# Optimization experiments

Measured on AMD Instinct MI355X. Metric: run time of the kernel, lower is better.

The kernel has to match this reference:

```python
import jax, jax.numpy as jnp
import numpy as np

B, T, F = 512, 1024, 8
H1, H2 = 70, 21   # '80k' config, bidirectional
D1, D2 = 30, 20


def _u(key, shape, fan):
    s = 1.0 / np.sqrt(fan)
    return jax.random.uniform(key, shape, jnp.float32, -s, s)


def setup_inputs() -> dict:
    key = jax.random.key(0)
    ks = iter(jax.random.split(key, 32))
    inp = {"x": jax.random.normal(next(ks), (B, T, F), jnp.float32)}
    # LSTM layer 1 (input F -> H1), forward and backward directions; torch gate order i,f,g,o
    for d in ("f", "b"):
        inp[f"w_ih1_{d}"] = _u(next(ks), (4 * H1, F), H1)
        inp[f"w_hh1_{d}"] = _u(next(ks), (4 * H1, H1), H1)
        inp[f"b_ih1_{d}"] = _u(next(ks), (4 * H1,), H1)
        inp[f"b_hh1_{d}"] = _u(next(ks), (4 * H1,), H1)
    # LSTM layer 2 (input 2*H1 -> H2)
    for d in ("f", "b"):
        inp[f"w_ih2_{d}"] = _u(next(ks), (4 * H2, 2 * H1), H2)
        inp[f"w_hh2_{d}"] = _u(next(ks), (4 * H2, H2), H2)
        inp[f"b_ih2_{d}"] = _u(next(ks), (4 * H2,), H2)
        inp[f"b_hh2_{d}"] = _u(next(ks), (4 * H2,), H2)
    # Dense head: 2*H2 -> D1 -> D2 -> 1
    inp["d1_w"] = _u(next(ks), (D1, 2 * H2), 2 * H2)
    inp["d1_b"] = _u(next(ks), (D1,), 2 * H2)
    inp["d2_w"] = _u(next(ks), (D2, D1), D1)
    inp["d2_b"] = _u(next(ks), (D2,), D1)
    inp["out_w"] = _u(next(ks), (1, D2), D2)
    inp["out_b"] = _u(next(ks), (1,), D2)
    return inp


def _lstm_dir(x, w_ih, w_hh, b_ih, b_hh, reverse):
    # x: [B, T, Fin]; torch LSTM gate order: i, f, g, o
    if reverse:
        x = x[:, ::-1]
    H = w_hh.shape[1]
    pre = jnp.einsum('btf,gf->btg', x, w_ih) + b_ih + b_hh  # [B, T, 4H]
    pre_t = jnp.moveaxis(pre, 1, 0)                          # [T, B, 4H]

    def step(carry, p):
        h, c = carry
        g = p + h @ w_hh.T
        i, f, gg, o = jnp.split(g, 4, axis=-1)
        c = jax.nn.sigmoid(f) * c + jax.nn.sigmoid(i) * jnp.tanh(gg)
        h = jax.nn.sigmoid(o) * jnp.tanh(c)
        return (h, c), h

    init = (jnp.zeros((x.shape[0], H), x.dtype), jnp.zeros((x.shape[0], H), x.dtype))
    _, hs = jax.lax.scan(step, init, pre_t)
    hs = jnp.moveaxis(hs, 0, 1)  # [B, T, H]
    if reverse:
        hs = hs[:, ::-1]
    return hs


def _bilstm(x, wf, uf, bif, bhf, wb, ub, bib, bhb):
    return jnp.concatenate([
        _lstm_dir(x, wf, uf, bif, bhf, reverse=False),
        _lstm_dir(x, wb, ub, bib, bhb, reverse=True),
    ], axis=-1)


def reference(x,
              w_ih1_f, w_hh1_f, b_ih1_f, b_hh1_f,
              w_ih1_b, w_hh1_b, b_ih1_b, b_hh1_b,
              w_ih2_f, w_hh2_f, b_ih2_f, b_hh2_f,
              w_ih2_b, w_hh2_b, b_ih2_b, b_hh2_b,
              d1_w, d1_b, d2_w, d2_b, out_w, out_b):
    h = _bilstm(x, w_ih1_f, w_hh1_f, b_ih1_f, b_hh1_f,
                w_ih1_b, w_hh1_b, b_ih1_b, b_hh1_b)   # [B, T, 2*H1]
    h = _bilstm(h, w_ih2_f, w_hh2_f, b_ih2_f, b_hh2_f,
                w_ih2_b, w_hh2_b, b_ih2_b, b_hh2_b)   # [B, T, 2*H2]
    h = jax.nn.relu(h @ d1_w.T + d1_b)
    h = jax.nn.relu(h @ d2_w.T + d2_b)
    return h @ out_w.T + out_b                          # [B, T, 1]
```

## Files before the change

### kernel.cpp

```cpp
#include <hip/hip_runtime.h>


typedef _Float16 v2f16 __attribute__((ext_vector_type(2)));
typedef _Float16 v4h   __attribute__((ext_vector_type(4)));
typedef _Float16 v8h   __attribute__((ext_vector_type(8)));
typedef float    f32x4 __attribute__((ext_vector_type(4)));

__device__ __forceinline__ float fdot2(v2f16 a, v2f16 b, float c) {
  return __builtin_amdgcn_fdot2(a, b, c, false);
}
#if __has_builtin(__builtin_amdgcn_rcpf)
__device__ __forceinline__ float rcpf(float x) { return __builtin_amdgcn_rcpf(x); }
#else
__device__ __forceinline__ float rcpf(float x) { return 1.f / x; }
#endif
__device__ __forceinline__ float ex2(float v) {
#if __has_builtin(__builtin_amdgcn_exp2f)
  return __builtin_amdgcn_exp2f(v);
#else
  return __expf(v * 0.6931471805599453f);
#endif
}
__device__ __forceinline__ float dpp_xor1(float v) {
  return __builtin_bit_cast(float,
      __builtin_amdgcn_update_dpp(0, __builtin_bit_cast(int, v),
                                  0xB1 , 0xF, 0xF, true));
}

__device__ __forceinline__ void lds_barrier() {
  asm volatile("s_waitcnt lgkmcnt(0)" ::: "memory");
  __builtin_amdgcn_s_barrier();
  __builtin_amdgcn_sched_barrier(0);
}

#define LOG2E  1.4426950408889634f
#define LOG2E2 2.8853900817779268f

#define O_W1M  0u
#define O_WP2  110592u
#define O_W2M  118656u
#define O_BIAS 177792u
#define O_DATA 178496u

__global__ void pack_kernel(const float* __restrict__ wihf, const float* __restrict__ whhf,
                            const float* __restrict__ wihb, const float* __restrict__ whhb,
                            const float* __restrict__ b1if, const float* __restrict__ b1hf,
                            const float* __restrict__ b1ib, const float* __restrict__ b1hb,
                            const float* __restrict__ wih2f, const float* __restrict__ wih2b,
                            const float* __restrict__ whh2f, const float* __restrict__ whh2b,
                            const float* __restrict__ bif, const float* __restrict__ bhf,
                            const float* __restrict__ bib, const float* __restrict__ bhb,
                            char* __restrict__ ws) {
  _Float16* w1m = (_Float16*)(ws + O_W1M);
  _Float16* wp2 = (_Float16*)(ws + O_WP2);
  _Float16* w2m = (_Float16*)(ws + O_W2M);
  float* biasc = (float*)(ws + O_BIAS);
  int idx = blockIdx.x * 256 + threadIdx.x;
  if (idx < 55296) {
    int d = idx / 27648, rem = idx % 27648, rp = rem / 96, k = rem % 96;
    int u = rp >> 2, g = rp & 3;
    const float* wih = d ? wihb : wihf;
    const float* whh = d ? whhb : whhf;
    const float* bi = d ? b1ib : b1if;
    const float* bh = d ? b1hb : b1hf;
    float v = 0.f;
    if (u < 70) {
      int src = g * 70 + u;
      float scale = (g == 2) ? LOG2E2 : LOG2E;
      if (k < 8) v = wih[src * 8 + k] * scale;
      else if (k < 78) v = whh[src * 70 + (k - 8)] * scale;
      else if (k == 78) v = (bi[src] + bh[src]) * scale;
    }
    w1m[idx] = (_Float16)v;
  } else if (idx < 59328) {
    int j = idx - 55296;
    int d = j / 2016, rem = j % 2016, r = rem / 24, k = rem % 24;
    const float* whh = d ? whh2b : whh2f;
    float scale = (r / 21 == 2) ? LOG2E2 : LOG2E;
    wp2[j] = (_Float16)((k < 21) ? whh[r * 21 + k] * scale : 0.f);
  } else if (idx < 88896) {
    int j = idx - 59328;
    int n = j / 168, k = j % 168;
    float v = 0.f;
    if (n < 168 && k < 140) {
      int d = n / 84, m = n % 84, u = m >> 2, g = m & 3;
      const float* wih = d ? wih2b : wih2f;
      float scale = (g == 2) ? LOG2E2 : LOG2E;
      v = wih[(g * 21 + u) * 140 + k] * scale;
    }
    w2m[j] = (_Float16)v;
  } else if (idx < 89072) {
    int n = idx - 88896;
    float v = 0.f;
    if (n < 168) {
      int d = n / 84, m = n % 84, u = m >> 2, g = m & 3;
      const float* bi = d ? bib : bif;
      const float* bh = d ? bhb : bhf;
      float scale = (g == 2) ? LOG2E2 : LOG2E;
      v = (bi[g * 21 + u] + bh[g * 21 + u]) * scale;
    }
    biasc[n] = v;
  }
}

__global__ __launch_bounds__(1024) void lstm1_kernel(
    const float* __restrict__ x,
    const _Float16* __restrict__ w1m,
    _Float16* __restrict__ h1, int b0, int nb) {
  __shared__ __align__(16) _Float16 km[2][16][104];
  const int tid = threadIdx.x;
  const int w = tid >> 6, lane = tid & 63;
  const int q = lane >> 4, bc = lane & 15;
  const int d = blockIdx.y;
  const int blg = blockIdx.x * 16;
  const int gb0 = b0 + blg;

  for (int i = tid; i < 2 * 16 * 104; i += 1024) ((_Float16*)km)[i] = (_Float16)0.f;

  const bool ldr = (w == 15);
  const bool two = (w < 2) || (w == 14);
  const int T0 = (w < 2) ? 2 * w : (w == 14 ? 16 : w + 2);

  v8h af[2][3];
  if (!ldr) {
#pragma unroll
    for (int kc = 0; kc < 3; ++kc)
      af[0][kc] = *(const v8h*)&w1m[(size_t)(d * 288 + T0 * 16 + bc) * 96 + kc * 32 + q * 8];
    if (two) {
#pragma unroll
      for (int kc = 0; kc < 3; ++kc)
        af[1][kc] = *(const v8h*)&w1m[(size_t)(d * 288 + (T0 + 1) * 16 + bc) * 96 + kc * 32 + q * 8];
    }
  }

  __syncthreads();

  if (tid < 16) {
    km[0][tid][78] = (_Float16)1.f;
    km[1][tid][78] = (_Float16)1.f;
  }
  const bool xlane = ldr && (lane < 32);
  const int xb = lane >> 1, xhalf = lane & 1;
  float4 xa, xb4, xc, xd;
  const float* xp = nullptr;
  const ptrdiff_t xstep = d ? -8 : 8;
  if (xlane) {
    const float* xrow = &x[((size_t)(gb0 + xb) * 1024) * 8 + xhalf * 4];
    int t0 = d ? 1023 : 0;
    float4 xv = *(const float4*)&xrow[(size_t)t0 * 8];
    v4h xh; xh[0] = (_Float16)xv.x; xh[1] = (_Float16)xv.y;
    xh[2] = (_Float16)xv.z; xh[3] = (_Float16)xv.w;
    *(v4h*)&km[0][xb][xhalf * 4] = xh;
    xa  = *(const float4*)&xrow[(size_t)(d ? 1022 : 1) * 8];
    xb4 = *(const float4*)&xrow[(size_t)(d ? 1021 : 2) * 8];
    xc  = *(const float4*)&xrow[(size_t)(d ? 1020 : 3) * 8];
    xd  = *(const float4*)&xrow[(size_t)(d ? 1019 : 4) * 8];
    xp  = &xrow[(size_t)(d ? 1018 : 5) * 8];
  }
  float c0 = 0.f, c1 = 0.f;
  int s = 0;
  __syncthreads();

#define GATE(Ai, ci, U)                                                      \
    {                                                                        \
      float ei = ex2(-Ai[0]);                                                \
      float ef = ex2(-Ai[1]);                                                \
      float eg = ex2(-Ai[2]);                                                \
      float eo = ex2(-Ai[3]);                                                \
      float sf = rcpf(1.f + ef);                                             \
      float ig = (1.f - eg) * rcpf((1.f + ei) * (1.f + eg));                 \
      ci = fmaf(sf, ci, ig);                                                 \
      float cl = fminf(fmaxf(ci, -14.f), 14.f);                              \
      float ec = ex2(cl * -LOG2E2);                                          \
      float hv = (1.f - ec) * rcpf((1.f + eo) * (1.f + ec));                 \
      if ((U) < 70) {                                                        \
        _Float16 hh = (_Float16)hv;                                          \
        km[nxt][bc][8 + (U)] = hh;                                           \
        h1[rowb + (U)] = hh;                                                 \
      }                                                                      \
    }

#define STEP1(XR)                                                            \
  {                                                                          \
    const int cur = s & 1, nxt = cur ^ 1;                                    \
    if (!ldr) {                                                              \
      v8h bf0 = *(const v8h*)&km[cur][bc][q * 8];                            \
      v8h bf1 = *(const v8h*)&km[cur][bc][32 + q * 8];                       \
      v8h bf2 = *(const v8h*)&km[cur][bc][64 + q * 8];                       \
      f32x4 z4 = (f32x4){0.f, 0.f, 0.f, 0.f};                                \
      f32x4 A0 = __builtin_amdgcn_mfma_f32_16x16x32_f16(af[0][0], bf0, z4, 0, 0, 0); \
      f32x4 A1 = z4;                                                         \
      if (two) A1 = __builtin_amdgcn_mfma_f32_16x16x32_f16(af[1][0], bf0, z4, 0, 0, 0); \
      A0 = __builtin_amdgcn_mfma_f32_16x16x32_f16(af[0][1], bf1, A0, 0, 0, 0); \
      if (two) A1 = __builtin_amdgcn_mfma_f32_16x16x32_f16(af[1][1], bf1, A1, 0, 0, 0); \
      A0 = __builtin_amdgcn_mfma_f32_16x16x32_f16(af[0][2], bf2, A0, 0, 0, 0); \
      if (two) A1 = __builtin_amdgcn_mfma_f32_16x16x32_f16(af[1][2], bf2, A1, 0, 0, 0); \
      const int te = d ? (1023 - s) : s;                                     \
      const size_t rowb = ((size_t)te * nb + blg + bc) * 176 + d * 70;       \
      GATE(A0, c0, T0 * 4 + q)                                               \
      if (two) GATE(A1, c1, (T0 + 1) * 4 + q)                                \
    } else if (xlane) {                                                      \
      if (s < 1023) {                                                        \
        v4h xh; xh[0] = (_Float16)XR.x; xh[1] = (_Float16)XR.y;              \
        xh[2] = (_Float16)XR.z; xh[3] = (_Float16)XR.w;                      \
        *(v4h*)&km[nxt][xb][xhalf * 4] = xh;                                 \
      }                                                                      \
      if (s <= 1018) XR = *(const float4*)xp;                                \
      xp += xstep;                                                           \
    }                                                                        \
    ++s;                                                                     \
    lds_barrier();                                                           \
  }

#pragma unroll 1
  for (int it = 0; it < 256; ++it) {
    STEP1(xa)
    STEP1(xb4)
    STEP1(xc)
    STEP1(xd)
  }
#undef STEP1
#undef GATE
}

__global__ __launch_bounds__(256) void pre2_kernel(
    _Float16* __restrict__ h1, const char* __restrict__ ws) {
  const _Float16* w2m = (const _Float16*)(ws + O_W2M);
  const float* biasc = (const float*)(ws + O_BIAS);
  __shared__ _Float16 Al[64][184];
  __shared__ float Bl[176];
  const int tid = threadIdx.x;
  const int r0 = blockIdx.x * 64;
#pragma unroll
  for (int i = 0; i < 6; ++i) {
    int cid = i * 256 + tid;
    if (cid < 1408) {
      int row = cid / 22, ch = cid % 22;
      *(v8h*)&Al[row][ch * 8] = *(const v8h*)&h1[(size_t)(r0 + row) * 176 + ch * 8];
    }
  }
  if (tid < 176) Bl[tid] = biasc[tid];
  __syncthreads();

  const int wv = tid >> 6, lane = tid & 63;
  const int ml = lane & 15, kq = lane >> 4;
  v8h af[5];
#pragma unroll
  for (int k = 0; k < 4; ++k)
    af[k] = *(const v8h*)&Al[wv * 16 + ml][k * 32 + kq * 8];
  {
    v8h a4 = *(const v8h*)&Al[wv * 16 + ml][128 + kq * 8];
    if (kq >= 2) {
#pragma unroll
      for (int j = 0; j < 8; ++j) a4[j] = (_Float16)0.f;
    } else if (kq == 1) {
#pragma unroll
      for (int j = 4; j < 8; ++j) a4[j] = (_Float16)0.f;
    }
    af[4] = a4;
  }

  const v8h* wg = (const v8h*)w2m;
  f32x4 acc[11];
#pragma unroll
  for (int ct = 0; ct < 11; ++ct) acc[ct] = (f32x4){0.f, 0.f, 0.f, 0.f};

  v8h bc[5], bn[5];
#pragma unroll
  for (int k = 0; k < 5; ++k) bn[k] = wg[(size_t)ml * 21 + k * 4 + kq];
#pragma unroll
  for (int ct = 0; ct < 11; ++ct) {
#pragma unroll
    for (int k = 0; k < 5; ++k) bc[k] = bn[k];
    if (ct < 10) {
#pragma unroll
      for (int k = 0; k < 5; ++k) bn[k] = wg[(size_t)((ct + 1) * 16 + ml) * 21 + k * 4 + kq];
    }
#pragma unroll
    for (int k = 0; k < 5; ++k)
      acc[ct] = __builtin_amdgcn_mfma_f32_16x16x32_f16(af[k], bc[k], acc[ct], 0, 0, 0);
  }
  __syncthreads();
#pragma unroll
  for (int ct = 0; ct < 11; ++ct) {
#pragma unroll
    for (int r = 0; r < 4; ++r) {
      int row = wv * 16 + kq * 4 + r, col = ct * 16 + ml;
      Al[row][col] = (_Float16)(acc[ct][r] + Bl[col]);
    }
  }
  __syncthreads();
#pragma unroll
  for (int i = 0; i < 6; ++i) {
    int cid = i * 256 + tid;
    if (cid < 1408) {
      int row = cid / 22, ch = cid % 22;
      *(v8h*)&h1[(size_t)(r0 + row) * 176 + ch * 8] = *(const v8h*)&Al[row][ch * 8];
    }
  }
}

__global__ __launch_bounds__(64) void lstm2_kernel(
    const _Float16* __restrict__ pre2, const _Float16* __restrict__ wp2,
    _Float16* __restrict__ h2, int nb) {
  __shared__ __align__(16) _Float16 kv[2][32];
  const int lane = threadIdx.x;
  const int bl = blockIdx.x;
  const int d = blockIdx.y;
  const int u = lane >> 1, p = lane & 1;
  const bool active = lane < 42;

  ((_Float16*)kv)[lane] = (_Float16)0.f;

  v2f16 w0[12], w1[12];
  if (active) {
    const v8h* wr0 = (const v8h*)&wp2[(d * 84 + (2 * p) * 21 + u) * 24];
    const v8h* wr1 = (const v8h*)&wp2[(d * 84 + (2 * p + 1) * 21 + u) * 24];
#pragma unroll
    for (int ch = 0; ch < 3; ++ch) {
      v8h a = wr0[ch], b = wr1[ch];
#pragma unroll
      for (int q = 0; q < 4; ++q) {
        v2f16 t0; t0[0] = a[2 * q]; t0[1] = a[2 * q + 1]; w0[ch * 4 + q] = t0;
        v2f16 t1; t1[0] = b[2 * q]; t1[1] = b[2 * q + 1]; w1[ch * 4 + q] = t1;
      }
    }
  }
  const int cp = d * 84 + u * 4 + 2 * p;
  const ptrdiff_t dlt = (ptrdiff_t)(d ? -nb : nb) * 176;
  const _Float16* pp = pre2 + ((size_t)(d ? 1023 : 0) * (size_t)nb + bl) * 176;

  v2f16 pa = *(const v2f16*)(pp + cp);
  v2f16 pb = *(const v2f16*)(pp + dlt + cp);
  v2f16 pc = *(const v2f16*)(pp + 2 * dlt + cp);
  v2f16 pd = *(const v2f16*)(pp + 3 * dlt + cp);
  v2f16 pe = *(const v2f16*)(pp + 4 * dlt + cp);
  v2f16 pg = *(const v2f16*)(pp + 5 * dlt + cp);
  v2f16 ph = *(const v2f16*)(pp + 6 * dlt + cp);
  v2f16 pi = *(const v2f16*)(pp + 7 * dlt + cp);
  const _Float16* pf = pp + 8 * dlt;

  float cc = 0.f;
  int s = 0;

#define L2STEP(P)                                                           \
  {                                                                         \
    const int cur = s & 1, nxt = cur ^ 1;                                   \
    float A0v = (float)P[0], A1v = (float)P[1];                             \
    const float4* kp = (const float4*)&kv[cur][0];                          \
    float4 q0 = kp[0], q1 = kp[1], q2 = kp[2];                              \
    __builtin_amdgcn_s_setprio(1);                                          \
    float x0 = A0v, x1 = 0.f, x2 = 0.f, x3 = 0.f;                           \
    float z0 = A1v, z1 = 0.f, z2 = 0.f, z3 = 0.f;                           \
    x0 = fdot2(__builtin_bit_cast(v2f16, q0.x), w0[0], x0);                 \
    x1 = fdot2(__builtin_bit_cast(v2f16, q0.y), w0[1], x1);                 \
    x2 = fdot2(__builtin_bit_cast(v2f16, q0.z), w0[2], x2);                 \
    x3 = fdot2(__builtin_bit_cast(v2f16, q0.w), w0[3], x3);                 \
    x0 = fdot2(__builtin_bit_cast(v2f16, q1.x), w0[4], x0);                 \
    x1 = fdot2(__builtin_bit_cast(v2f16, q1.y), w0[5], x1);                 \
    x2 = fdot2(__builtin_bit_cast(v2f16, q1.z), w0[6], x2);                 \
    x3 = fdot2(__builtin_bit_cast(v2f16, q1.w), w0[7], x3);                 \
    x0 = fdot2(__builtin_bit_cast(v2f16, q2.x), w0[8], x0);                 \
    x1 = fdot2(__builtin_bit_cast(v2f16, q2.y), w0[9], x1);                 \
    x2 = fdot2(__builtin_bit_cast(v2f16, q2.z), w0[10], x2);                \
    x3 = fdot2(__builtin_bit_cast(v2f16, q2.w), w0[11], x3);                \
    z0 = fdot2(__builtin_bit_cast(v2f16, q0.x), w1[0], z0);                 \
    z1 = fdot2(__builtin_bit_cast(v2f16, q0.y), w1[1], z1);                 \
    z2 = fdot2(__builtin_bit_cast(v2f16, q0.z), w1[2], z2);                 \
    z3 = fdot2(__builtin_bit_cast(v2f16, q0.w), w1[3], z3);                 \
    z0 = fdot2(__builtin_bit_cast(v2f16, q1.x), w1[4], z0);                 \
    z1 = fdot2(__builtin_bit_cast(v2f16, q1.y), w1[5], z1);                 \
    z2 = fdot2(__builtin_bit_cast(v2f16, q1.z), w1[6], z2);                 \
    z3 = fdot2(__builtin_bit_cast(v2f16, q1.w), w1[7], z3);                 \
    z0 = fdot2(__builtin_bit_cast(v2f16, q2.x), w1[8], z0);                 \
    z1 = fdot2(__builtin_bit_cast(v2f16, q2.y), w1[9], z1);                 \
    z2 = fdot2(__builtin_bit_cast(v2f16, q2.z), w1[10], z2);                \
    z3 = fdot2(__builtin_bit_cast(v2f16, q2.w), w1[11], z3);                \
    float A = (x0 + x1) + (x2 + x3), Bv = (z0 + z1) + (z2 + z3);            \
            \
    float r0v = rcpf(1.f + ex2(-A));                                        \
    float Y0 = p ? fmaf(2.f, r0v, -1.f) : r0v;                              \
    float Y1 = rcpf(1.f + ex2(-Bv));                                        \
    float Zs = dpp_xor1(Y0);                                                \
    float Ws = dpp_xor1(Y1);                                                \
    float ai = p ? Zs : Y0;                                                 \
    float af = p ? Ws : Y1;                                                 \
    float ag = p ? Y0 : Zs;                                                 \
    float ao = p ? Y1 : Ws;                                                 \
    cc = fmaf(af, cc, ai * ag);                                             \
    float tc = fmaf(2.f, rcpf(1.f + ex2(cc * -LOG2E2)), -1.f);              \
    float hv = ao * tc;                                                     \
    __builtin_amdgcn_s_setprio(0);                                          \
    if (active && p == 0) {                                                 \
      _Float16 hh = (_Float16)hv;                                           \
      int te = d ? (1023 - s) : s;                                          \
      kv[nxt][u] = hh;                                                      \
      h2[((size_t)te * nb + bl) * 48 + d * 21 + u] = hh;                    \
    }                                                                       \
    if (s < 1016) P = *(const v2f16*)(pf + cp);                             \
    pf += dlt;                                                              \
    ++s;                                                                    \
  }

#pragma unroll 1
  for (int it = 0; it < 128; ++it) {
    L2STEP(pa)
    L2STEP(pb)
    L2STEP(pc)
    L2STEP(pd)
    L2STEP(pe)
    L2STEP(pg)
    L2STEP(ph)
    L2STEP(pi)
  }
#undef L2STEP
}

__global__ __launch_bounds__(256) void head_kernel(
    const _Float16* __restrict__ h2,
    const float* __restrict__ d1w, const float* __restrict__ d1b,
    const float* __restrict__ d2w, const float* __restrict__ d2b,
    const float* __restrict__ ow, const float* __restrict__ ob,
    float* __restrict__ out, int b0, int lognb) {
  int n = blockIdx.x * 256 + threadIdx.x;
  int t = n >> lognb, bl = n & ((1 << lognb) - 1);
  const v8h* hp = (const v8h*)&h2[(size_t)n * 48];
  float in[48];
#pragma unroll
  for (int i = 0; i < 6; ++i) {
    v8h hc = hp[i];
#pragma unroll
    for (int j = 0; j < 8; ++j) in[i * 8 + j] = (float)hc[j];
  }
  float a1[30];
#pragma unroll
  for (int cc = 0; cc < 30; ++cc) {
    float a = d1b[cc];
#pragma unroll
    for (int k = 0; k < 42; ++k) a += in[k] * d1w[cc * 42 + k];
    a1[cc] = fmaxf(a, 0.f);
  }
  float a2[20];
#pragma unroll
  for (int cc = 0; cc < 20; ++cc) {
    float a = d2b[cc];
#pragma unroll
    for (int k = 0; k < 30; ++k) a += a1[k] * d2w[cc * 30 + k];
    a2[cc] = fmaxf(a, 0.f);
  }
  float o = ob[0];
#pragma unroll
  for (int k = 0; k < 20; ++k) o += a2[k] * ow[k];
  out[(size_t)(b0 + bl) * 1024 + t] = o;
}

extern "C" void kernel_launch(void* const* d_in, const int* in_sizes, int n_in,
                              void* d_out, int out_size, void* d_ws, size_t ws_size,
                              hipStream_t stream) {
  const float* x = (const float*)d_in[0];
  const float* wih1f = (const float*)d_in[1];
  const float* whh1f = (const float*)d_in[2];
  const float* bih1f = (const float*)d_in[3];
  const float* bhh1f = (const float*)d_in[4];
  const float* wih1b = (const float*)d_in[5];
  const float* whh1b = (const float*)d_in[6];
  const float* bih1b = (const float*)d_in[7];
  const float* bhh1b = (const float*)d_in[8];
  const float* wih2f = (const float*)d_in[9];
  const float* whh2f = (const float*)d_in[10];
  const float* bih2f = (const float*)d_in[11];
  const float* bhh2f = (const float*)d_in[12];
  const float* wih2b = (const float*)d_in[13];
  const float* whh2b = (const float*)d_in[14];
  const float* bih2b = (const float*)d_in[15];
  const float* bhh2b = (const float*)d_in[16];
  const float* d1w = (const float*)d_in[17];
  const float* d1b = (const float*)d_in[18];
  const float* d2w = (const float*)d_in[19];
  const float* d2b = (const float*)d_in[20];
  const float* ow = (const float*)d_in[21];
  const float* ob = (const float*)d_in[22];
  float* out = (float*)d_out;
  char* wsb = (char*)d_ws;

  const int cands[6] = {1, 2, 4, 8, 16, 32};
  int nslice = 32;
  for (int i = 0; i < 6; ++i) {
    size_t rows = (size_t)(512 / cands[i]) * 1024;
    if (O_DATA + rows * 448 <= ws_size) { nslice = cands[i]; break; }
  }
  const int nb = 512 / nslice;
  int lognb = 0; while ((1 << lognb) < nb) ++lognb;
  const size_t rows = (size_t)nb * 1024;

  _Float16* w1m = (_Float16*)(wsb + O_W1M);
  _Float16* wp2 = (_Float16*)(wsb + O_WP2);
  _Float16* h1  = (_Float16*)(wsb + O_DATA);
  _Float16* h2  = (_Float16*)(wsb + O_DATA + rows * 352);

  pack_kernel<<<348, 256, 0, stream>>>(wih1f, whh1f, wih1b, whh1b,
                                       bih1f, bhh1f, bih1b, bhh1b,
                                       wih2f, wih2b, whh2f, whh2b,
                                       bih2f, bhh2f, bih2b, bhh2b, wsb);

  for (int s = 0; s < nslice; ++s) {
    const int b0 = s * nb;
    lstm1_kernel<<<dim3(nb / 16, 2), 1024, 0, stream>>>(x, w1m, h1, b0, nb);
    pre2_kernel<<<nb * 16, 256, 0, stream>>>(h1, wsb);
    lstm2_kernel<<<dim3(nb, 2), 64, 0, stream>>>(h1, wp2, h2, nb);
    head_kernel<<<nb * 4, 256, 0, stream>>>(h2, d1w, d1b, d2w, d2b, ow, ob,
                                            out, b0, lognb);
  }
}
```

Measured before the change: 1.199 ms.

## Fuse layer-2 input projection into layer-1 recurrence via atomic fp16 accumulation

```diff
diff --git a/kernel.cpp b/kernel.cpp
--- a/kernel.cpp
+++ b/kernel.cpp
@@ -1,4 +1,5 @@
 #include <hip/hip_runtime.h>
+#include <hip/hip_fp16.h>
 
 
 typedef _Float16 v2f16 __attribute__((ext_vector_type(2)));
@@ -26,6 +27,10 @@
       __builtin_amdgcn_update_dpp(0, __builtin_bit_cast(int, v),
                                   0xB1 , 0xF, 0xF, true));
 }
+__device__ __forceinline__ void atom_pk_add(_Float16* p, float v0, float v1) {
+  v2f16 t; t[0] = (_Float16)v0; t[1] = (_Float16)v1;
+  unsafeAtomicAdd(reinterpret_cast<__half2*>(p), __builtin_bit_cast(__half2, t));
+}
 
 __device__ __forceinline__ void lds_barrier() {
   asm volatile("s_waitcnt lgkmcnt(0)" ::: "memory");
@@ -38,9 +43,9 @@
 
 #define O_W1M  0u
 #define O_WP2  110592u
-#define O_W2M  118656u
-#define O_BIAS 177792u
-#define O_DATA 178496u
+#define O_W2F  118656u
+#define O_BIAS 186240u
+#define O_DATA 186944u
 
 __global__ void pack_kernel(const float* __restrict__ wihf, const float* __restrict__ whhf,
                             const float* __restrict__ wihb, const float* __restrict__ whhb,
@@ -53,7 +58,7 @@
                             char* __restrict__ ws) {
   _Float16* w1m = (_Float16*)(ws + O_W1M);
   _Float16* wp2 = (_Float16*)(ws + O_WP2);
-  _Float16* w2m = (_Float16*)(ws + O_W2M);
+  _Float16* w2f = (_Float16*)(ws + O_W2F);
   float* biasc = (float*)(ws + O_BIAS);
   int idx = blockIdx.x * 256 + threadIdx.x;
   if (idx < 55296) {
@@ -78,19 +83,19 @@
     const float* whh = d ? whh2b : whh2f;
     float scale = (r / 21 == 2) ? LOG2E2 : LOG2E;
     wp2[j] = (_Float16)((k < 21) ? whh[r * 21 + k] * scale : 0.f);
-  } else if (idx < 88896) {
+  } else if (idx < 93120) {
     int j = idx - 59328;
-    int n = j / 168, k = j % 168;
+    int dd = j / 16896, rem = j % 16896, n = rem / 96, k = rem % 96;
     float v = 0.f;
-    if (n < 168 && k < 140) {
-      int d = n / 84, m = n % 84, u = m >> 2, g = m & 3;
-      const float* wih = d ? wih2b : wih2f;
+    if (n < 168 && k >= 8 && k < 78) {
+      int d2 = n / 84, m = n % 84, u = m >> 2, g = m & 3;
+      const float* wih = d2 ? wih2b : wih2f;
       float scale = (g == 2) ? LOG2E2 : LOG2E;
-      v = wih[(g * 21 + u) * 140 + k] * scale;
-    }
-    w2m[j] = (_Float16)v;
-  } else if (idx < 89072) {
-    int n = idx - 88896;
+      v = wih[(g * 21 + u) * 140 + dd * 70 + (k - 8)] * scale;
+    }
+    w2f[j] = (_Float16)v;
+  } else if (idx < 93296) {
+    int n = idx - 93120;
     float v = 0.f;
     if (n < 168) {
       int d = n / 84, m = n % 84, u = m >> 2, g = m & 3;
@@ -106,7 +111,9 @@
 __global__ __launch_bounds__(1024) void lstm1_kernel(
     const float* __restrict__ x,
     const _Float16* __restrict__ w1m,
-    _Float16* __restrict__ h1, int b0, int nb) {
+    const _Float16* __restrict__ w2f,
+    const float* __restrict__ biasc,
+    _Float16* __restrict__ pre, int b0, int nb) {
   __shared__ __align__(16) _Float16 km[2][16][104];
   const int tid = threadIdx.x;
   const int w = tid >> 6, lane = tid & 63;
@@ -130,6 +137,22 @@
 #pragma unroll
       for (int kc = 0; kc < 3; ++kc)
         af[1][kc] = *(const v8h*)&w1m[(size_t)(d * 288 + (T0 + 1) * 16 + bc) * 96 + kc * 32 + q * 8];
+    }
+  }
+
+  const bool w2w = (w >= 2 && w <= 12);
+  const int Tw = w - 2;
+  const int n0 = Tw * 16 + q * 4;
+  const bool w2st = w2w && (n0 < 168);
+  v8h wf0, wf1, wf2;
+  f32x4 pbias = (f32x4){0.f, 0.f, 0.f, 0.f};
+  if (w2w) {
+    wf0 = *(const v8h*)&w2f[(size_t)(d * 176 + Tw * 16 + bc) * 96 + 0 * 32 + q * 8];
+    wf1 = *(const v8h*)&w2f[(size_t)(d * 176 + Tw * 16 + bc) * 96 + 1 * 32 + q * 8];
+    wf2 = *(const v8h*)&w2f[(size_t)(d * 176 + Tw * 16 + bc) * 96 + 2 * 32 + q * 8];
+    if (d == 0 && n0 < 168) {
+      pbias[0] = biasc[n0];     pbias[1] = biasc[n0 + 1];
+      pbias[2] = biasc[n0 + 2]; pbias[3] = biasc[n0 + 3];
     }
   }
 
@@ -173,11 +196,7 @@
       float cl = fminf(fmaxf(ci, -14.f), 14.f);                              \
       float ec = ex2(cl * -LOG2E2);                                          \
       float hv = (1.f - ec) * rcpf((1.f + eo) * (1.f + ec));                 \
-      if ((U) < 70) {                                                        \
-        _Float16 hh = (_Float16)hv;                                          \
-        km[nxt][bc][8 + (U)] = hh;                                           \
-        h1[rowb + (U)] = hh;                                                 \
-      }                                                                      \
+      if ((U) < 70) km[nxt][bc][8 + (U)] = (_Float16)hv;                     \
     }
 
 #define STEP1(XR)                                                            \
@@ -195,8 +214,16 @@
       if (two) A1 = __builtin_amdgcn_mfma_f32_16x16x32_f16(af[1][1], bf1, A1, 0, 0, 0); \
       A0 = __builtin_amdgcn_mfma_f32_16x16x32_f16(af[0][2], bf2, A0, 0, 0, 0); \
       if (two) A1 = __builtin_amdgcn_mfma_f32_16x16x32_f16(af[1][2], bf2, A1, 0, 0, 0); \
-      const int te = d ? (1023 - s) : s;                                     \
-      const size_t rowb = ((size_t)te * nb + blg + bc) * 176 + d * 70;       \
+      if (w2st && s > 0) {             \
+        f32x4 Pv = pbias;                                                    \
+        Pv = __builtin_amdgcn_mfma_f32_16x16x32_f16(wf0, bf0, Pv, 0, 0, 0);  \
+        Pv = __builtin_amdgcn_mfma_f32_16x16x32_f16(wf1, bf1, Pv, 0, 0, 0);  \
+        Pv = __builtin_amdgcn_mfma_f32_16x16x32_f16(wf2, bf2, Pv, 0, 0, 0);  \
+        int tp = d ? (1024 - s) : (s - 1);                                   \
+        _Float16* pq = &pre[((size_t)tp * nb + blg + bc) * 176 + n0];        \
+        atom_pk_add(pq, Pv[0], Pv[1]);                                       \
+        atom_pk_add(pq + 2, Pv[2], Pv[3]);                                   \
+      }                                                                      \
       GATE(A0, c0, T0 * 4 + q)                                               \
       if (two) GATE(A1, c1, (T0 + 1) * 4 + q)                                \
     } else if (xlane) {                                                      \
@@ -221,82 +248,19 @@
   }
 #undef STEP1
 #undef GATE
-}
-
-__global__ __launch_bounds__(256) void pre2_kernel(
-    _Float16* __restrict__ h1, const char* __restrict__ ws) {
-  const _Float16* w2m = (const _Float16*)(ws + O_W2M);
-  const float* biasc = (const float*)(ws + O_BIAS);
-  __shared__ _Float16 Al[64][184];
-  __shared__ float Bl[176];
-  const int tid = threadIdx.x;
-  const int r0 = blockIdx.x * 64;
-#pragma unroll
-  for (int i = 0; i < 6; ++i) {
-    int cid = i * 256 + tid;
-    if (cid < 1408) {
-      int row = cid / 22, ch = cid % 22;
-      *(v8h*)&Al[row][ch * 8] = *(const v8h*)&h1[(size_t)(r0 + row) * 176 + ch * 8];
-    }
-  }
-  if (tid < 176) Bl[tid] = biasc[tid];
-  __syncthreads();
-
-  const int wv = tid >> 6, lane = tid & 63;
-  const int ml = lane & 15, kq = lane >> 4;
-  v8h af[5];
-#pragma unroll
-  for (int k = 0; k < 4; ++k)
-    af[k] = *(const v8h*)&Al[wv * 16 + ml][k * 32 + kq * 8];
-  {
-    v8h a4 = *(const v8h*)&Al[wv * 16 + ml][128 + kq * 8];
-    if (kq >= 2) {
-#pragma unroll
-      for (int j = 0; j < 8; ++j) a4[j] = (_Float16)0.f;
-    } else if (kq == 1) {
-#pragma unroll
-      for (int j = 4; j < 8; ++j) a4[j] = (_Float16)0.f;
-    }
-    af[4] = a4;
-  }
-
-  const v8h* wg = (const v8h*)w2m;
-  f32x4 acc[11];
-#pragma unroll
-  for (int ct = 0; ct < 11; ++ct) acc[ct] = (f32x4){0.f, 0.f, 0.f, 0.f};
-
-  v8h bc[5], bn[5];
-#pragma unroll
-  for (int k = 0; k < 5; ++k) bn[k] = wg[(size_t)ml * 21 + k * 4 + kq];
-#pragma unroll
-  for (int ct = 0; ct < 11; ++ct) {
-#pragma unroll
-    for (int k = 0; k < 5; ++k) bc[k] = bn[k];
-    if (ct < 10) {
-#pragma unroll
-      for (int k = 0; k < 5; ++k) bn[k] = wg[(size_t)((ct + 1) * 16 + ml) * 21 + k * 4 + kq];
-    }
-#pragma unroll
-    for (int k = 0; k < 5; ++k)
-      acc[ct] = __builtin_amdgcn_mfma_f32_16x16x32_f16(af[k], bc[k], acc[ct], 0, 0, 0);
-  }
-  __syncthreads();
-#pragma unroll
-  for (int ct = 0; ct < 11; ++ct) {
-#pragma unroll
-    for (int r = 0; r < 4; ++r) {
-      int row = wv * 16 + kq * 4 + r, col = ct * 16 + ml;
-      Al[row][col] = (_Float16)(acc[ct][r] + Bl[col]);
-    }
-  }
-  __syncthreads();
-#pragma unroll
-  for (int i = 0; i < 6; ++i) {
-    int cid = i * 256 + tid;
-    if (cid < 1408) {
-      int row = cid / 22, ch = cid % 22;
-      *(v8h*)&h1[(size_t)(r0 + row) * 176 + ch * 8] = *(const v8h*)&Al[row][ch * 8];
-    }
+
+  if (w2st) {
+    v8h bf0 = *(const v8h*)&km[0][bc][q * 8];
+    v8h bf1 = *(const v8h*)&km[0][bc][32 + q * 8];
+    v8h bf2 = *(const v8h*)&km[0][bc][64 + q * 8];
+    f32x4 Pv = pbias;
+    Pv = __builtin_amdgcn_mfma_f32_16x16x32_f16(wf0, bf0, Pv, 0, 0, 0);
+    Pv = __builtin_amdgcn_mfma_f32_16x16x32_f16(wf1, bf1, Pv, 0, 0, 0);
+    Pv = __builtin_amdgcn_mfma_f32_16x16x32_f16(wf2, bf2, Pv, 0, 0, 0);
+    int tp = d ? 0 : 1023;
+    _Float16* pq = &pre[((size_t)tp * nb + blg + bc) * 176 + n0];
+    atom_pk_add(pq, Pv[0], Pv[1]);
+    atom_pk_add(pq + 2, Pv[2], Pv[3]);
   }
 }
 
@@ -495,19 +459,22 @@
 
   _Float16* w1m = (_Float16*)(wsb + O_W1M);
   _Float16* wp2 = (_Float16*)(wsb + O_WP2);
-  _Float16* h1  = (_Float16*)(wsb + O_DATA);
+  _Float16* w2f = (_Float16*)(wsb + O_W2F);
+  const float* biasc = (const float*)(wsb + O_BIAS);
+  _Float16* pre = (_Float16*)(wsb + O_DATA);
   _Float16* h2  = (_Float16*)(wsb + O_DATA + rows * 352);
 
-  pack_kernel<<<348, 256, 0, stream>>>(wih1f, whh1f, wih1b, whh1b,
+  pack_kernel<<<365, 256, 0, stream>>>(wih1f, whh1f, wih1b, whh1b,
                                        bih1f, bhh1f, bih1b, bhh1b,
                                        wih2f, wih2b, whh2f, whh2b,
                                        bih2f, bhh2f, bih2b, bhh2b, wsb);
 
   for (int s = 0; s < nslice; ++s) {
     const int b0 = s * nb;
-    lstm1_kernel<<<dim3(nb / 16, 2), 1024, 0, stream>>>(x, w1m, h1, b0, nb);
-    pre2_kernel<<<nb * 16, 256, 0, stream>>>(h1, wsb);
-    lstm2_kernel<<<dim3(nb, 2), 64, 0, stream>>>(h1, wp2, h2, nb);
+    (void)hipMemsetAsync(pre, 0, rows * 352, stream);
+    lstm1_kernel<<<dim3(nb / 16, 2), 1024, 0, stream>>>(x, w1m, w2f, biasc,
+                                                        pre, b0, nb);
+    lstm2_kernel<<<dim3(nb, 2), 64, 0, stream>>>(pre, wp2, h2, nb);
     head_kernel<<<nb * 4, 256, 0, stream>>>(h2, d1w, d1b, d2w, d2b, ow, ob,
                                             out, b0, lognb);
   }
```

Result: slower. 1.784 ms (+48.9%).
